# Performance work log

Hardware: AMD Instinct MI355X
Metric: run time of the kernel (lower is better)

Reference implementation:

```python
import jax, jax.numpy as jnp
import numpy as np

HID, PROJ, ATTN = 512, 1024, 128
B, L = 4, 2048


def _apply_rope(x):
    # x: [B, L, 2, ATTN]; RoPE over sequence dim (axis=1)
    half = x.shape[-1] // 2
    inv_freq = jnp.power(10000.0, -jnp.arange(half, dtype=jnp.float32) / half)
    pos = jnp.arange(x.shape[1], dtype=x.dtype)
    sinusoid = pos[:, None] * inv_freq.astype(x.dtype)          # [L, half]
    sin = jnp.sin(sinusoid)[None, :, None, :]                   # [1, L, 1, half]
    cos = jnp.cos(sinusoid)[None, :, None, :]
    x1, x2 = jnp.split(x, 2, axis=-1)
    return jnp.concatenate([x1 * cos - x2 * sin, x2 * cos + x1 * sin], axis=-1)


def setup_inputs() -> dict:
    key = jax.random.key(0)
    ks = jax.random.split(key, 8)
    node = jax.random.normal(ks[0], (B, L, HID), dtype=jnp.float32)
    bias = jax.random.normal(ks[1], (B, L, L), dtype=jnp.float32)
    scaling = jnp.full((1,), ATTN ** -0.5, dtype=jnp.float32)
    w1 = jax.random.normal(ks[2], (HID, 2 * PROJ + ATTN), dtype=jnp.float32) * (HID ** -0.5)
    b1 = jnp.zeros((2 * PROJ + ATTN,), dtype=jnp.float32)
    ms_weight = jax.random.normal(ks[3], (2, ATTN), dtype=jnp.float32) * 0.02
    ms_bias = jnp.zeros((2, ATTN), dtype=jnp.float32)
    w2 = jax.random.normal(ks[4], (PROJ, HID), dtype=jnp.float32) * (PROJ ** -0.5)
    b2 = jnp.zeros((HID,), dtype=jnp.float32)
    return {"node": node, "bias": bias, "scaling": scaling, "w1": w1, "b1": b1,
            "ms_weight": ms_weight, "ms_bias": ms_bias, "w2": w2, "b2": b2}


def reference(node, bias, scaling, w1, b1, ms_weight, ms_bias, w2, b2):
    # gated projection + SiLU
    gva = jax.nn.silu(node @ w1 + b1)                           # [B, L, 2P+A]
    gates, values, base = jnp.split(gva, [PROJ, 2 * PROJ], axis=-1)
    # multi-headed scaling -> [B, L, 2, A], then RoPE, then split q/k
    qk = base[..., None, :] * ms_weight + ms_bias               # [B, L, 2, A]
    qk = _apply_rope(qk)
    q, k = qk[..., 0, :], qk[..., 1, :]                         # [B, L, A]
    logits = jnp.einsum('bid,bjd->bij', q * scaling, k) + bias  # [B, L, L]
    attn = jax.nn.softmax(logits, axis=-1)
    out = jnp.einsum('bij,bjd->bid', attn, values)              # [B, L, P]
    return (out * gates) @ w2 + b2                              # [B, L, HID]
```

## Files before the change

### kernel.cpp

```cpp
#include <hip/hip_runtime.h>
#include <math.h>

#define HIDN 512
#define PROJ 1024
#define ATTN 128
#define BATCH 4
#define SEQ 2048
#define N1 (2*PROJ+ATTN)
#define ROWS (BATCH*SEQ)
#define QR 16

typedef __attribute__((ext_vector_type(4))) float f32x4;
typedef __attribute__((ext_vector_type(8))) short bf16x8;

__device__ __forceinline__ short f2bf(float x){
    unsigned u = __builtin_bit_cast(unsigned, x);
    unsigned rounding = 0x7fffu + ((u >> 16) & 1u);
    u += rounding;
    return (short)(u >> 16);
}
__device__ __forceinline__ float bf2f(short s){
    unsigned u = ((unsigned)(unsigned short)s) << 16;
    return __builtin_bit_cast(float, u);
}

__device__ __forceinline__ void gload16(const void* g, void* l){
    __builtin_amdgcn_global_load_lds((const __attribute__((address_space(1))) void*)g,
                                     (__attribute__((address_space(3))) void*)l,
                                     16, 0, 0);
}

template<int BK, class Epi>
__device__ __forceinline__ void gemm_bt_tile(const short* __restrict__ A, int lda,
                                             const short* __restrict__ BT, int ldb,
                                             int m0, int n0, int K, Epi epi)
{
    __shared__ __align__(16) short lA[2][128*BK];
    __shared__ __align__(16) short lB[2][128*BK];
    const int t = threadIdx.x;
    const int lane = t & 63;
    const int w = t >> 6;
    const int wr = (w >> 1) * 64, wc = (w & 1) * 64;
    const int half = lane >> 4, l16 = lane & 15;
    constexpr int SPT = BK/16;

    f32x4 acc[4][4];
    #pragma unroll
    for (int i=0;i<4;i++)
        #pragma unroll
        for (int j=0;j<4;j++)
            acc[i][j] = (f32x4){0.f,0.f,0.f,0.f};

    auto stage = [&](int buf, int k0){
        #pragma unroll
        for (int i = 0; i < SPT; i++) {
            int li = i*256 + t;
            int r = li / (BK/8), s = li % (BK/8);
            int ss = (BK==64) ? (s ^ (r & 7)) : (s ^ ((r >> 1) & 3));
            gload16(A + (size_t)(m0+r)*lda + k0 + ss*8, lA[buf] + li*8);
        }
        #pragma unroll
        for (int i = 0; i < SPT; i++) {
            int li = i*256 + t;
            int r = li / (BK/8), s = li % (BK/8);
            int ss = (BK==64) ? (s ^ (r & 7)) : (s ^ ((r >> 1) & 3));
            gload16(BT + (size_t)(n0+r)*ldb + k0 + ss*8, lB[buf] + li*8);
        }
    };

    stage(0, 0);
    __syncthreads();
    int cur = 0;
    for (int k0 = BK; k0 <= K; k0 += BK) {
        if (k0 < K) stage(cur^1, k0);
        #pragma unroll
        for (int kk = 0; kk < BK; kk += 32) {
            bf16x8 af[4], bfr[4];
            const int cs = (kk >> 3) + half;
            #pragma unroll
            for (int i=0;i<4;i++){
                int row = wr + i*16 + l16;
                int sl = (BK==64) ? (cs ^ (row & 7)) : (cs ^ ((row >> 1) & 3));
                af[i] = *(const bf16x8*)(lA[cur] + row*BK + sl*8);
            }
            #pragma unroll
            for (int j=0;j<4;j++){
                int row = wc + j*16 + l16;
                int sl = (BK==64) ? (cs ^ (row & 7)) : (cs ^ ((row >> 1) & 3));
                bfr[j] = *(const bf16x8*)(lB[cur] + row*BK + sl*8);
            }
            #pragma unroll
            for (int i=0;i<4;i++)
                #pragma unroll
                for (int j=0;j<4;j++)
                    acc[i][j] = __builtin_amdgcn_mfma_f32_16x16x32_bf16(af[i], bfr[j], acc[i][j], 0, 0, 0);
        }
        __syncthreads();
        cur ^= 1;
    }
    #pragma unroll
    for (int i=0;i<4;i++)
        #pragma unroll
        for (int j=0;j<4;j++)
            #pragma unroll
            for (int q=0;q<4;q++)
                epi(m0 + wr + i*16 + half*4 + q, n0 + wc + j*16 + l16, acc[i][j][q]);
}

__global__ void k_cast_node(const float* __restrict__ in, short* __restrict__ out){
    int idx = blockIdx.x*256 + threadIdx.x;
    const float4 v = ((const float4*)in)[idx];
    short4 o; o.x = f2bf(v.x); o.y = f2bf(v.y); o.z = f2bf(v.z); o.w = f2bf(v.w);
    ((short4*)out)[idx] = o;
}

__global__ void k_transpose_cast(const float* __restrict__ in, short* __restrict__ out,
                                 int R, int C){
    __shared__ short tile[64][65];
    int r0 = blockIdx.y*64, c0 = blockIdx.x*64;
    int t = threadIdx.x;
    #pragma unroll
    for (int i=0;i<16;i++){
        int lin = i*256 + t; int r = lin>>6, c = lin&63;
        tile[r][c] = f2bf(in[(size_t)(r0+r)*C + c0+c]);
    }
    __syncthreads();
    #pragma unroll
    for (int i=0;i<16;i++){
        int lin = i*256 + t; int c = lin>>6, r = lin&63;
        out[(size_t)(c0+c)*R + r0+r] = tile[r][c];
    }
}

__global__ void k_transpose_v(const short* __restrict__ values, short* __restrict__ VT){
    __shared__ short tile[64][65];
    int z = blockIdx.z;
    int c0 = blockIdx.x*64, r0 = blockIdx.y*64;
    int t = threadIdx.x;
    #pragma unroll
    for (int i=0;i<16;i++){
        int lin = i*256 + t; int r = lin>>6, c = lin&63;
        tile[r][c] = values[(size_t)(z*SEQ + r0+r)*PROJ + c0+c];
    }
    __syncthreads();
    #pragma unroll
    for (int i=0;i<16;i++){
        int lin = i*256 + t; int c = lin>>6, r = lin&63;
        VT[((size_t)z*PROJ + c0+c)*SEQ + r0+r] = tile[r][c];
    }
}

__global__ __launch_bounds__(256) void k_mm1(const short* __restrict__ nodeb,
        const short* __restrict__ w1T, const float* __restrict__ b1,
        short* __restrict__ gates, short* __restrict__ values, short* __restrict__ baseb){
    int b = blockIdx.x;
    int wg = (b & 7) * (N1/128*64/8) + (b >> 3);
    int n0 = (wg % (N1/128))*128, m0 = (wg / (N1/128))*128;
    gemm_bt_tile<32>(nodeb, HIDN, w1T, HIDN, m0, n0, HIDN,
        [=](int row, int col, float v){
            v += b1[col];
            v = v / (1.f + __expf(-v));
            short bv = f2bf(v);
            if (col < PROJ)        gates [(size_t)row*PROJ + col]        = bv;
            else if (col < 2*PROJ) values[(size_t)row*PROJ + col-PROJ]   = bv;
            else                   baseb [(size_t)row*ATTN + col-2*PROJ] = bv;
        });
}

__global__ void k_rope2(const short* __restrict__ baseb, const float* __restrict__ msw,
                        const float* __restrict__ msb, const float* __restrict__ scaling,
                        short* __restrict__ qb, short* __restrict__ kb){
    int idx = blockIdx.x*256 + threadIdx.x;
    int d = idx & 63;
    int row = idx >> 6;
    int l = row & (SEQ-1);
    float inv = exp2f(-(float)d * (13.287712379549449f/64.f));
    float ang = (float)l * inv;
    float s = sinf(ang), c = cosf(ang);
    const short* bp = baseb + (size_t)row*ATTN;
    float b_lo = bf2f(bp[d]), b_hi = bf2f(bp[d+64]);
    float x1q = b_lo*msw[d]        + msb[d];
    float x2q = b_hi*msw[d+64]     + msb[d+64];
    float x1k = b_lo*msw[128+d]    + msb[128+d];
    float x2k = b_hi*msw[128+d+64] + msb[128+d+64];
    float sc = scaling[0];
    qb[(size_t)row*ATTN + d]    = f2bf((x1q*c - x2q*s)*sc);
    qb[(size_t)row*ATTN + d+64] = f2bf((x2q*c + x1q*s)*sc);
    kb[(size_t)row*ATTN + d]    = f2bf(x1k*c - x2k*s);
    kb[(size_t)row*ATTN + d+64] = f2bf(x2k*c + x1k*s);
}

__global__ __launch_bounds__(512, 4) void k_qksm(
        const short* __restrict__ qg, const short* __restrict__ kg,
        const float* __restrict__ bias, short* __restrict__ P,
        float* __restrict__ linv)
{
    __shared__ short ptw[8][16][56];
    __shared__ float s_l[8][16];

    const int z = blockIdx.y;
    const int r0 = blockIdx.x * QR;
    const int t = threadIdx.x;
    const int w = t >> 6;
    const int lane = t & 63;
    const int l16 = lane & 15, half = lane >> 4;

    const short* Q  = qg + ((size_t)z*SEQ + r0)*ATTN;
    const short* K  = kg + (size_t)z*SEQ*ATTN;
    const float* Bb = bias + ((size_t)z*SEQ + r0)*SEQ;
    short* Pp = P + ((size_t)z*SEQ + r0)*SEQ;

    bf16x8 qf[4];
    #pragma unroll
    for (int kc=0;kc<4;kc++)
        qf[kc] = *(const bf16x8*)(Q + (size_t)l16*ATTN + kc*32 + half*8);

    f32x4 ts = (f32x4){0.f,0.f,0.f,0.f};

    float bn[2][4];
    #pragma unroll
    for (int j=0;j<2;j++)
        #pragma unroll
        for (int e=0;e<4;e++)
            bn[j][e] = Bb[(size_t)(half*4+e)*SEQ + w*32 + j*16 + l16];

    #pragma unroll 2
    for (int c=0; c<8; c++){
        float bx[2][4];
        if (c < 7){
            #pragma unroll
            for (int j=0;j<2;j++)
                #pragma unroll
                for (int e=0;e<4;e++)
                    bx[j][e] = Bb[(size_t)(half*4+e)*SEQ + (c+1)*256 + w*32 + j*16 + l16];
        }
        #pragma unroll
        for (int j=0;j<2;j++){
            const int kvb = c*256 + w*32 + j*16;
            const short* Kc = K + (size_t)(kvb + l16)*ATTN;
            f32x4 a = (f32x4){bn[j][0], bn[j][1], bn[j][2], bn[j][3]};
            #pragma unroll
            for (int kc=0;kc<4;kc++){
                bf16x8 kf = *(const bf16x8*)(Kc + kc*32 + half*8);
                a = __builtin_amdgcn_mfma_f32_16x16x32_bf16(qf[kc], kf, a, 0,0,0);
            }
            float p0 = __expf(a[0]), p1 = __expf(a[1]);
            float p2 = __expf(a[2]), p3 = __expf(a[3]);
            ts[0] += p0; ts[1] += p1; ts[2] += p2; ts[3] += p3;
            ptw[w][half*4+0][j*16+l16] = f2bf(p0);
            ptw[w][half*4+1][j*16+l16] = f2bf(p1);
            ptw[w][half*4+2][j*16+l16] = f2bf(p2);
            ptw[w][half*4+3][j*16+l16] = f2bf(p3);
        }
        {
            bf16x8 v = *(const bf16x8*)&ptw[w][lane>>2][(lane&3)*8];
            *(bf16x8*)(Pp + (size_t)(lane>>2)*SEQ + c*256 + w*32 + (lane&3)*8) = v;
        }
        #pragma unroll
        for (int j=0;j<2;j++)
            #pragma unroll
            for (int e=0;e<4;e++)
                bn[j][e] = bx[j][e];
    }

    #pragma unroll
    for (int e=0;e<4;e++){
        ts[e] += __shfl_xor(ts[e],1,64);
        ts[e] += __shfl_xor(ts[e],2,64);
        ts[e] += __shfl_xor(ts[e],4,64);
        ts[e] += __shfl_xor(ts[e],8,64);
    }
    if (l16 == 0){
        #pragma unroll
        for (int e=0;e<4;e++) s_l[w][half*4+e] = ts[e];
    }
    __syncthreads();
    if (t < 16){
        float sum = 0.f;
        #pragma unroll
        for (int ww=0; ww<8; ww++) sum += s_l[ww][t];
        linv[(size_t)z*SEQ + r0 + t] = 1.f/sum;
    }
}

__global__ __launch_bounds__(256) void k_pv2(const short* __restrict__ P,
        const short* __restrict__ VT, const short* __restrict__ gates,
        const float* __restrict__ linv, short* __restrict__ a2){
    int b = blockIdx.x;
    int wg = (b & 7) * 64 + (b >> 3);
    int xx = wg & 7, yy = (wg >> 3) & 15, z = wg >> 7;
    const short* A = P  + (size_t)z*SEQ*SEQ;
    const short* B = VT + (size_t)z*PROJ*SEQ;
    int n0 = xx*128, m0 = yy*128;
    gemm_bt_tile<64>(A, SEQ, B, SEQ, m0, n0, SEQ,
        [=](int r, int c, float v){
            size_t gi = ((size_t)z*SEQ + r)*PROJ + c;
            a2[gi] = f2bf(v * linv[(size_t)z*SEQ + r] * bf2f(gates[gi]));
        });
}

__global__ __launch_bounds__(256) void k_mm2(const short* __restrict__ a2,
        const short* __restrict__ w2T, const float* __restrict__ b2,
        float* __restrict__ out){
    int b = blockIdx.x;
    int wg = (b & 7) * 32 + (b >> 3);
    int n0 = (wg & 3)*128, m0 = (wg >> 2)*128;
    gemm_bt_tile<32>(a2, PROJ, w2T, PROJ, m0, n0, PROJ,
        [=](int r, int c, float v){
            out[(size_t)r*HIDN + c] = v + b2[c];
        });
}

extern "C" void kernel_launch(void* const* d_in, const int* in_sizes, int n_in,
                              void* d_out, int out_size, void* d_ws, size_t ws_size,
                              hipStream_t stream) {
    const float* node    = (const float*)d_in[0];
    const float* bias    = (const float*)d_in[1];
    const float* scaling = (const float*)d_in[2];
    const float* w1      = (const float*)d_in[3];
    const float* b1      = (const float*)d_in[4];
    const float* msw     = (const float*)d_in[5];
    const float* msb     = (const float*)d_in[6];
    const float* w2      = (const float*)d_in[7];
    const float* b2      = (const float*)d_in[8];
    float* out = (float*)d_out;

    char* p = (char*)d_ws;
    auto alloc = [&](size_t bytes){ char* r = p; p += (bytes + 255) & ~(size_t)255; return r; };
    short* nodeb  = (short*)alloc((size_t)ROWS*HIDN*2);
    short* w1T    = (short*)alloc((size_t)N1*HIDN*2);
    short* w2T    = (short*)alloc((size_t)HIDN*PROJ*2);
    short* gates  = (short*)alloc((size_t)ROWS*PROJ*2);
    short* values = (short*)alloc((size_t)ROWS*PROJ*2);
    short* VT     = (short*)alloc((size_t)BATCH*PROJ*SEQ*2);
    short* baseb  = (short*)alloc((size_t)ROWS*ATTN*2);
    short* qb     = (short*)alloc((size_t)ROWS*ATTN*2);
    short* kb     = (short*)alloc((size_t)ROWS*ATTN*2);
    short* Pbuf   = (short*)alloc((size_t)BATCH*SEQ*SEQ*2);
    float* linv   = (float*)alloc((size_t)ROWS*4);
    short* a2buf  = (short*)alloc((size_t)ROWS*PROJ*2);

    k_cast_node<<<ROWS*HIDN/1024, 256, 0, stream>>>(node, nodeb);
    k_transpose_cast<<<dim3(N1/64, HIDN/64), 256, 0, stream>>>(w1, w1T, HIDN, N1);
    k_transpose_cast<<<dim3(HIDN/64, PROJ/64), 256, 0, stream>>>(w2, w2T, PROJ, HIDN);
    k_mm1<<<(N1/128)*(ROWS/128), 256, 0, stream>>>(nodeb, w1T, b1, gates, values, baseb);
    k_transpose_v<<<dim3(PROJ/64, SEQ/64, BATCH), 256, 0, stream>>>(values, VT);
    k_rope2<<<ROWS*64/256, 256, 0, stream>>>(baseb, msw, msb, scaling, qb, kb);
    k_qksm<<<dim3(SEQ/QR, BATCH), 512, 0, stream>>>(qb, kb, bias, Pbuf, linv);
    k_pv2<<<(PROJ/128)*(SEQ/128)*BATCH, 256, 0, stream>>>(Pbuf, VT, gates, linv, a2buf);
    k_mm2<<<(HIDN/128)*(ROWS/128), 256, 0, stream>>>(a2buf, w2T, b2, out);
}
```

Measured before the change: 164.8 us.

## Retile QK-softmax into 128x128 LDS-staged tiles with split row-sum combine

The QK^T+bias+exp kernel now works on 128x128 (query, key) tiles per 256-thread block. Q and K are staged into swizzled LDS with async global-to-LDS loads, so each K row is reused across 128 query rows instead of being reread from global per 16-row block. Partial row sums are written per key tile and reduced by a new small combine kernel that produces the inverse normalizers. The MFMA is computed as K·Q^T with the bias loaded as float4 directly into the accumulators, and P is transposed through LDS for coalesced stores. This costs an extra launch and a 16x partial-sum buffer.

```diff
diff --git a/kernel.cpp b/kernel.cpp
--- a/kernel.cpp
+++ b/kernel.cpp
@@ -8,7 +8,6 @@
 #define SEQ 2048
 #define N1 (2*PROJ+ATTN)
 #define ROWS (BATCH*SEQ)
-#define QR 16
 
 typedef __attribute__((ext_vector_type(4))) float f32x4;
 typedef __attribute__((ext_vector_type(8))) short bf16x8;
@@ -190,97 +189,116 @@
     kb[(size_t)row*ATTN + d+64] = f2bf(x2k*c + x1k*s);
 }
 
-__global__ __launch_bounds__(512, 4) void k_qksm(
+__global__ __launch_bounds__(256) void k_qksm(
         const short* __restrict__ qg, const short* __restrict__ kg,
         const float* __restrict__ bias, short* __restrict__ P,
-        float* __restrict__ linv)
+        float* __restrict__ lsum16)
 {
-    __shared__ short ptw[8][16][56];
-    __shared__ float s_l[8][16];
-
-    const int z = blockIdx.y;
-    const int r0 = blockIdx.x * QR;
+    __shared__ __align__(16) short smem[32768];
+    __shared__ float sl[2][128];
+
+    const int b = blockIdx.x;
+    const int wg = (b & 7) * 128 + (b >> 3);
+    const int z  = wg >> 8;
+    const int qt = (wg >> 4) & 15;
+    const int kt = wg & 15;
+    const int q0 = qt * 128, kv0 = kt * 128;
+
     const int t = threadIdx.x;
-    const int w = t >> 6;
-    const int lane = t & 63;
-    const int l16 = lane & 15, half = lane >> 4;
-
-    const short* Q  = qg + ((size_t)z*SEQ + r0)*ATTN;
-    const short* K  = kg + (size_t)z*SEQ*ATTN;
-    const float* Bb = bias + ((size_t)z*SEQ + r0)*SEQ;
-    short* Pp = P + ((size_t)z*SEQ + r0)*SEQ;
-
-    bf16x8 qf[4];
-    #pragma unroll
-    for (int kc=0;kc<4;kc++)
-        qf[kc] = *(const bf16x8*)(Q + (size_t)l16*ATTN + kc*32 + half*8);
-
-    f32x4 ts = (f32x4){0.f,0.f,0.f,0.f};
-
-    float bn[2][4];
-    #pragma unroll
-    for (int j=0;j<2;j++)
-        #pragma unroll
-        for (int e=0;e<4;e++)
-            bn[j][e] = Bb[(size_t)(half*4+e)*SEQ + w*32 + j*16 + l16];
-
-    #pragma unroll 2
-    for (int c=0; c<8; c++){
-        float bx[2][4];
-        if (c < 7){
-            #pragma unroll
-            for (int j=0;j<2;j++)
-                #pragma unroll
-                for (int e=0;e<4;e++)
-                    bx[j][e] = Bb[(size_t)(half*4+e)*SEQ + (c+1)*256 + w*32 + j*16 + l16];
-        }
-        #pragma unroll
-        for (int j=0;j<2;j++){
-            const int kvb = c*256 + w*32 + j*16;
-            const short* Kc = K + (size_t)(kvb + l16)*ATTN;
-            f32x4 a = (f32x4){bn[j][0], bn[j][1], bn[j][2], bn[j][3]};
-            #pragma unroll
-            for (int kc=0;kc<4;kc++){
-                bf16x8 kf = *(const bf16x8*)(Kc + kc*32 + half*8);
-                a = __builtin_amdgcn_mfma_f32_16x16x32_bf16(qf[kc], kf, a, 0,0,0);
-            }
-            float p0 = __expf(a[0]), p1 = __expf(a[1]);
-            float p2 = __expf(a[2]), p3 = __expf(a[3]);
-            ts[0] += p0; ts[1] += p1; ts[2] += p2; ts[3] += p3;
-            ptw[w][half*4+0][j*16+l16] = f2bf(p0);
-            ptw[w][half*4+1][j*16+l16] = f2bf(p1);
-            ptw[w][half*4+2][j*16+l16] = f2bf(p2);
-            ptw[w][half*4+3][j*16+l16] = f2bf(p3);
-        }
-        {
-            bf16x8 v = *(const bf16x8*)&ptw[w][lane>>2][(lane&3)*8];
-            *(bf16x8*)(Pp + (size_t)(lane>>2)*SEQ + c*256 + w*32 + (lane&3)*8) = v;
-        }
-        #pragma unroll
-        for (int j=0;j<2;j++)
-            #pragma unroll
-            for (int e=0;e<4;e++)
-                bn[j][e] = bx[j][e];
-    }
-
-    #pragma unroll
-    for (int e=0;e<4;e++){
-        ts[e] += __shfl_xor(ts[e],1,64);
-        ts[e] += __shfl_xor(ts[e],2,64);
-        ts[e] += __shfl_xor(ts[e],4,64);
-        ts[e] += __shfl_xor(ts[e],8,64);
-    }
-    if (l16 == 0){
-        #pragma unroll
-        for (int e=0;e<4;e++) s_l[w][half*4+e] = ts[e];
-    }
-    __syncthreads();
-    if (t < 16){
-        float sum = 0.f;
-        #pragma unroll
-        for (int ww=0; ww<8; ww++) sum += s_l[ww][t];
-        linv[(size_t)z*SEQ + r0 + t] = 1.f/sum;
-    }
+    const int lane = t & 63, w = t >> 6;
+    const int wr = (w >> 1)*64, wc = (w & 1)*64;
+    const int half = lane >> 4, l16 = lane & 15;
+
+    const short* Kg = kg + ((size_t)z*SEQ + kv0)*ATTN;
+    const short* Qg = qg + ((size_t)z*SEQ + q0)*ATTN;
+
+    #pragma unroll
+    for (int i = 0; i < 8; i++) {
+        int li = i*256 + t;
+        int r = li >> 4, s = li & 15;
+        int ss = s ^ (r & 15);
+        gload16(Kg + (size_t)r*ATTN + ss*8, smem + li*8);
+        gload16(Qg + (size_t)r*ATTN + ss*8, smem + 16384 + li*8);
+    }
+
+    f32x4 acc[4][4];
+    #pragma unroll
+    for (int i=0;i<4;i++)
+        #pragma unroll
+        for (int j=0;j<4;j++)
+            acc[i][j] = *(const f32x4*)(bias
+                + ((size_t)z*SEQ + q0 + wc + j*16 + l16)*SEQ
+                + kv0 + wr + i*16 + half*4);
+
+    __syncthreads();
+
+    #pragma unroll
+    for (int kk = 0; kk < 128; kk += 32) {
+        const int cs = (kk >> 3) + half;
+        bf16x8 af[4], bfr[4];
+        #pragma unroll
+        for (int i=0;i<4;i++){
+            int row = wr + i*16 + l16;
+            af[i] = *(const bf16x8*)(smem + row*128 + (cs ^ (row & 15))*8);
+        }
+        #pragma unroll
+        for (int j=0;j<4;j++){
+            int row = wc + j*16 + l16;
+            bfr[j] = *(const bf16x8*)(smem + 16384 + row*128 + (cs ^ (row & 15))*8);
+        }
+        #pragma unroll
+        for (int i=0;i<4;i++)
+            #pragma unroll
+            for (int j=0;j<4;j++)
+                acc[i][j] = __builtin_amdgcn_mfma_f32_16x16x32_bf16(af[i], bfr[j], acc[i][j], 0, 0, 0);
+    }
+
+    __syncthreads();
+
+    short* pt = smem;
+    float tsum[4];
+    #pragma unroll
+    for (int j=0;j<4;j++){
+        int col = wc + j*16 + l16;
+        float sj = 0.f;
+        #pragma unroll
+        for (int i=0;i<4;i++){
+            float p0=__expf(acc[i][j][0]), p1=__expf(acc[i][j][1]);
+            float p2=__expf(acc[i][j][2]), p3=__expf(acc[i][j][3]);
+            sj += p0+p1+p2+p3;
+            short4 pv; pv.x=f2bf(p0); pv.y=f2bf(p1); pv.z=f2bf(p2); pv.w=f2bf(p3);
+            *(short4*)(pt + col*136 + wr + i*16 + half*4) = pv;
+        }
+        tsum[j] = sj;
+    }
+    #pragma unroll
+    for (int j=0;j<4;j++){
+        tsum[j] += __shfl_xor(tsum[j],16,64);
+        tsum[j] += __shfl_xor(tsum[j],32,64);
+    }
+    if (half==0){
+        #pragma unroll
+        for (int j=0;j<4;j++) sl[wr>>6][wc + j*16 + l16] = tsum[j];
+    }
+    __syncthreads();
+
+    short* Pp = P + ((size_t)z*SEQ + q0)*SEQ + kv0;
+    #pragma unroll
+    for (int i=0;i<8;i++){
+        int idx = i*256 + t;
+        int q = idx >> 4, g = idx & 15;
+        *(bf16x8*)(Pp + (size_t)q*SEQ + g*8) = *(const bf16x8*)(pt + q*136 + g*8);
+    }
+    if (t < 128)
+        lsum16[(size_t)kt*ROWS + (size_t)z*SEQ + q0 + t] = sl[0][t] + sl[1][t];
+}
+
+__global__ void k_combine(const float* __restrict__ lsum16, float* __restrict__ linv){
+    int r = blockIdx.x*256 + threadIdx.x;
+    float s = 0.f;
+    #pragma unroll
+    for (int kt=0; kt<16; kt++) s += lsum16[(size_t)kt*ROWS + r];
+    linv[r] = 1.f/s;
 }
 
 __global__ __launch_bounds__(256) void k_pv2(const short* __restrict__ P,
@@ -294,8 +312,9 @@
     int n0 = xx*128, m0 = yy*128;
     gemm_bt_tile<64>(A, SEQ, B, SEQ, m0, n0, SEQ,
         [=](int r, int c, float v){
-            size_t gi = ((size_t)z*SEQ + r)*PROJ + c;
-            a2[gi] = f2bf(v * linv[(size_t)z*SEQ + r] * bf2f(gates[gi]));
+            size_t ri = (size_t)z*SEQ + r;
+            size_t gi = ri*PROJ + c;
+            a2[gi] = f2bf(v * linv[ri] * bf2f(gates[gi]));
         });
 }
 
@@ -337,6 +356,7 @@
     short* qb     = (short*)alloc((size_t)ROWS*ATTN*2);
     short* kb     = (short*)alloc((size_t)ROWS*ATTN*2);
     short* Pbuf   = (short*)alloc((size_t)BATCH*SEQ*SEQ*2);
+    float* lsum16 = (float*)alloc((size_t)16*ROWS*4);
     float* linv   = (float*)alloc((size_t)ROWS*4);
     short* a2buf  = (short*)alloc((size_t)ROWS*PROJ*2);
 
@@ -346,7 +366,8 @@
     k_mm1<<<(N1/128)*(ROWS/128), 256, 0, stream>>>(nodeb, w1T, b1, gates, values, baseb);
     k_transpose_v<<<dim3(PROJ/64, SEQ/64, BATCH), 256, 0, stream>>>(values, VT);
     k_rope2<<<ROWS*64/256, 256, 0, stream>>>(baseb, msw, msb, scaling, qb, kb);
-    k_qksm<<<dim3(SEQ/QR, BATCH), 512, 0, stream>>>(qb, kb, bias, Pbuf, linv);
+    k_qksm<<<16*16*BATCH, 256, 0, stream>>>(qb, kb, bias, Pbuf, lsum16);
+    k_combine<<<ROWS/256, 256, 0, stream>>>(lsum16, linv);
     k_pv2<<<(PROJ/128)*(SEQ/128)*BATCH, 256, 0, stream>>>(Pbuf, VT, gates, linv, a2buf);
     k_mm2<<<(HIDN/128)*(ROWS/128), 256, 0, stream>>>(a2buf, w2T, b2, out);
 }
```

New measurement: 152.2 us. 1.08x faster.
